# Performance work log

Measured on AMD Instinct MI355X. Metric: run time of the kernel, lower is better.

## Reference

```python
import jax, jax.numpy as jnp
import numpy as np

B, N, S, K = 32, 2048, 64, 128   # clouds, pts/cloud, fps centers (ratio=64/2048), max neighbors
R = 0.2                          # radius ball-query
SLOPE = 0.2                      # LeakyReLU negative slope
C_CONV = [3, 64, 128, 512]       # PointConv local nn
D_FEAT = 512


def leaky(x):
    return jnp.where(x >= 0, x, SLOPE * x)


def _init_linear(key, din, dout):
    kw, kb = jax.random.split(key)
    lim = 1.0 / np.sqrt(din)
    W = jax.random.uniform(kw, (din, dout), minval=-lim, maxval=lim, dtype=jnp.float32)
    b = jax.random.uniform(kb, (dout,), minval=-lim, maxval=lim, dtype=jnp.float32)
    return W, b


def setup_inputs() -> dict:
    key = jax.random.key(0)
    ks = jax.random.split(key, 6)
    pos = jax.random.uniform(ks[0], (B * N, 3), dtype=jnp.float32)
    batch = (jnp.arange(B * N, dtype=jnp.int32) // N)
    W1, b1 = _init_linear(ks[1], 3, 64)
    W2, b2 = _init_linear(ks[2], 64, 128)
    W3, b3 = _init_linear(ks[3], 128, 512)
    W4, b4 = _init_linear(ks[4], D_FEAT + 3, 512)
    W5, b5 = _init_linear(ks[5], 512, 1024)
    return {"pos": pos, "batch": batch,
            "W1": W1, "b1": b1, "W2": W2, "b2": b2, "W3": W3, "b3": b3,
            "W4": W4, "b4": b4, "W5": W5, "b5": b5}


def _fps_one(p):
    """Deterministic farthest point sampling on one cloud p:[N,3] -> idx:[S]."""
    d0 = jnp.sum((p - p[0]) ** 2, axis=-1)

    def step(dists, _):
        nxt = jnp.argmax(dists).astype(jnp.int32)
        dists = jnp.minimum(dists, jnp.sum((p - p[nxt]) ** 2, axis=-1))
        return dists, nxt

    _, rest = jax.lax.scan(step, d0, None, length=S - 1)
    return jnp.concatenate([jnp.zeros((1,), jnp.int32), rest])


def _encoder(pos, W1, b1, W2, b2, W3, b3, W4, b4, W5, b5):
    pts = pos.reshape(B, N, 3)
    idx = jax.vmap(_fps_one)(pts)                                   # [B,S] local fps indices
    centers = jnp.take_along_axis(pts, idx[:, :, None], axis=1)     # [B,S,3]

    # radius ball query (first-by-index up to K neighbors, like torch_cluster cap)
    d2 = jnp.sum((centers[:, :, None, :] - pts[:, None, :, :]) ** 2, axis=-1)  # [B,S,N]
    inball = d2 < R * R
    keys = jnp.where(inball, jnp.arange(N, dtype=jnp.int32)[None, None, :], N)
    nbr = jnp.sort(keys, axis=-1)[:, :, :K]                          # [B,S,K]
    valid = nbr < N
    nbr = jnp.where(valid, nbr, 0)

    # PointConv: gather relative positions -> MLP -> masked max aggregation
    nbr_pos = jnp.take_along_axis(pts[:, None, :, :], nbr[..., None], axis=2)  # [B,S,K,3]
    rel = nbr_pos - centers[:, :, None, :]
    h = leaky(rel @ W1 + b1)
    h = leaky(h @ W2 + b2)
    h = leaky(h @ W3 + b3)                                           # [B,S,K,512]
    h = jnp.where(valid[..., None], h, -jnp.inf)
    feat = jnp.max(h, axis=2)                                        # [B,S,512] (self always in ball)

    g = jnp.concatenate([feat, centers], axis=-1).reshape(B * S, D_FEAT + 3)
    g = leaky(g @ W4 + b4)
    out = g @ W5 + b5                                                # [B*S,1024]
    mean, logvar = out[:, :512], out[:, 512:]
    std = jnp.exp(0.5 * logvar)

    # global edge indices (x_idx = neighbor point id, y_idx = center id), -1 padded
    x_idx = jnp.where(valid, nbr + jnp.arange(B, dtype=jnp.int32)[:, None, None] * N, -1).reshape(-1)
    y_idx = jnp.where(valid, jnp.arange(B * S, dtype=jnp.int32).reshape(B, S, 1), -1).reshape(-1)
    return mean, std, x_idx, y_idx


def reference(pos, batch, W1, b1, W2, b2, W3, b3, W4, b4, W5, b5):
    # batch is implied by the fixed [B,N] layout (sorted, equal-size clouds)
    return _encoder(pos, W1, b1, W2, b2, W3, b3, W4, b4, W5, b5)
```

## Files before the change

kernel.cpp:

```cpp
#include <hip/hip_runtime.h>
#include <hip/hip_bf16.h>

#define NB 32
#define NP 2048
#define NS 64
#define NK 128

#define MEAN_OFF 0
#define STD_OFF  1048576
#define XIDX_OFF 2097152
#define YIDX_OFF 2359296

#define GA_LD 576

typedef __attribute__((ext_vector_type(4)))  short s4;
typedef __attribute__((ext_vector_type(8)))  short short8;
typedef __attribute__((ext_vector_type(16))) float f32x16;

static __device__ __forceinline__ float leaky(float x){ return x >= 0.0f ? x : 0.2f * x; }

static __device__ __forceinline__ unsigned short bf16u(float v){
    __hip_bfloat16 h = __float2bfloat16(v);
    return *(unsigned short*)&h;
}

static __device__ __forceinline__ unsigned cvtpk(float a, float b){
    unsigned d;
    asm("v_cvt_pk_bf16_f32 %0, %1, %2" : "=v"(d) : "v"(a), "v"(b));
    return d;
}
static __device__ __forceinline__ void plswap(unsigned &a, unsigned &b){
    asm volatile("v_permlane32_swap_b32 %0, %1" : "+v"(a), "+v"(b));
}

static __device__ __forceinline__ float d2s(float ax,float ay,float az,float bx,float by,float bz){
    float dx = __fsub_rn(ax,bx), dy = __fsub_rn(ay,by), dz = __fsub_rn(az,bz);
    return __fadd_rn(__fadd_rn(__fmul_rn(dx,dx),__fmul_rn(dy,dy)),__fmul_rn(dz,dz));
}

__global__ __launch_bounds__(256) void fps_prep_kernel(const float* __restrict__ pos,
                                                       float* __restrict__ centersWs,
                                                       const float* __restrict__ W2,
                                                       const float* __restrict__ W3,
                                                       const float* __restrict__ W4,
                                                       const float* __restrict__ W5,
                                                       __hip_bfloat16* __restrict__ W2T,
                                                       __hip_bfloat16* __restrict__ W3T,
                                                       __hip_bfloat16* __restrict__ W4T,
                                                       __hip_bfloat16* __restrict__ W5T)
{
    if (blockIdx.x >= NB) {
        int g = (blockIdx.x - NB)*256 + threadIdx.x;
        if (g < 65536) {
            int c = g >> 7, i = g & 127;
            int byte = c*256 + ((i*2) ^ ((c&15)<<4));
            W3T[byte>>1] = __float2bfloat16(W3[(size_t)i*512 + c]);
        }
        if (g < 8192) {
            int i = g >> 6, j = g & 63;
            W2T[g] = __float2bfloat16(W2[(size_t)j*128 + i]);
        }
        for (int e = g; e < 512*GA_LD; e += 131072) {
            int n = e / GA_LD, k = e - n*GA_LD;
            float v = (k < 515) ? W4[(size_t)k*512 + n] : 0.0f;
            W4T[e] = __float2bfloat16(v);
        }
        for (int e = g; e < 1024*512; e += 131072) {
            int n = e >> 9, k = e & 511;
            W5T[e] = __float2bfloat16(W5[(size_t)k*1024 + n]);
        }
        return;
    }

    int b = blockIdx.x;
    int t = threadIdx.x;
    __shared__ float px[NP], py[NP], pz[NP];
    __shared__ float redv[2][4];
    __shared__ int   redi[2][4];

    const float* pb = pos + (size_t)b * NP * 3;
    for (int n = t; n < NP; n += 256) {
        px[n] = pb[n*3+0]; py[n] = pb[n*3+1]; pz[n] = pb[n*3+2];
    }
    __syncthreads();

    float p0x = px[0], p0y = py[0], p0z = pz[0];
    float dl[8];
    #pragma unroll
    for (int q = 0; q < 8; q++) {
        int n = t + q*256;
        dl[q] = d2s(px[n],py[n],pz[n], p0x,p0y,p0z);
    }
    if (t == 0) {
        centersWs[(b*NS)*3+0] = p0x;
        centersWs[(b*NS)*3+1] = p0y;
        centersWs[(b*NS)*3+2] = p0z;
    }

    int w = t >> 6;
    for (int s = 1; s < NS; s++) {
        float bv = -1.0f; int bi = 0;
        #pragma unroll
        for (int q = 0; q < 8; q++) {
            int n = t + q*256;
            if (dl[q] > bv) { bv = dl[q]; bi = n; }
        }
        #pragma unroll
        for (int m = 32; m > 0; m >>= 1) {
            float ov = __shfl_xor(bv, m);
            int   oi = __shfl_xor(bi, m);
            if (ov > bv || (ov == bv && oi < bi)) { bv = ov; bi = oi; }
        }
        if ((t & 63) == 0) { redv[s&1][w] = bv; redi[s&1][w] = bi; }
        __syncthreads();
        float v = redv[s&1][0]; int j = redi[s&1][0];
        #pragma unroll
        for (int k = 1; k < 4; k++) {
            if (redv[s&1][k] > v || (redv[s&1][k] == v && redi[s&1][k] < j)) { v = redv[s&1][k]; j = redi[s&1][k]; }
        }
        float cx = px[j], cy = py[j], cz = pz[j];
        if (t == 0) {
            centersWs[(b*NS+s)*3+0] = cx;
            centersWs[(b*NS+s)*3+1] = cy;
            centersWs[(b*NS+s)*3+2] = cz;
        }
        #pragma unroll
        for (int q = 0; q < 8; q++) {
            int n = t + q*256;
            dl[q] = fminf(dl[q], d2s(px[n],py[n],pz[n], cx,cy,cz));
        }
    }
}

__global__ __launch_bounds__(256, 4) void ball_mlp_kernel(
    const float* __restrict__ pos,
    const float* __restrict__ W1, const float* __restrict__ b1,
    const float* __restrict__ b2, const float* __restrict__ b3,
    const __hip_bfloat16* __restrict__ W2Tp,
    const __hip_bfloat16* __restrict__ W3Tp,
    const float* __restrict__ centersWs,
    float* __restrict__ out,
    __hip_bfloat16* __restrict__ gAb)
{
    __shared__ char smem[37392];
    char*  h1s  = smem;
    float* relL = (float*)(smem + 32768);
    int*   nbL  = (int*)(smem + 32768);
    float* b2s  = (float*)(smem + 34816);
    float* b3s  = (float*)(smem + 35328);
    int*   cntW4= (int*)(smem + 37376);

    const short* W2T  = (const short*)W2Tp;
    const char*  W3Tb = (const char*)W3Tp;

    int r = blockIdx.x, b = r >> 6, tid = threadIdx.x;
    int l = tid & 63, w = tid >> 6;
    int l31 = l & 31;
    int hsel = l >> 5;
    int jsel8 = hsel * 8;
    int colsel = hsel * 16;

#define STAGE_W3(CH, DST)                                                                              \
    {                                                                                                  \
        const char* _s = W3Tb + (CH)*8192 + w*2048 + l*16;                                             \
        char* _d = (DST) + w*2048;                                                                     \
        __builtin_amdgcn_global_load_lds((const __attribute__((address_space(1))) void*)(_s),          \
                                         (__attribute__((address_space(3))) void*)(_d), 16, 0, 0);     \
        __builtin_amdgcn_global_load_lds((const __attribute__((address_space(1))) void*)(_s + 1024),   \
                                         (__attribute__((address_space(3))) void*)(_d + 1024), 16, 0, 0); \
    }

    STAGE_W3(0, smem + 16384);
    STAGE_W3(1, smem + 24576);

    float cx = centersWs[r*3+0], cy = centersWs[r*3+1], cz = centersWs[r*3+2];

    const float* pb = pos + (size_t)b * NP * 3;
    {
        int myCnt = 0;
        #pragma unroll
        for (int c = 0; c < 8; c++) {
            int n = w*512 + c*64 + l;
            float x = pb[n*3+0], y = pb[n*3+1], z = pb[n*3+2];
            bool in = d2s(cx,cy,cz, x,y,z) < 0.04f;
            unsigned long long m = __ballot(in);
            int before = __popcll(m & ((1ull << l) - 1ull));
            int p = myCnt + before;
            if (in && p < NK) nbL[w*NK + p] = n;
            myCnt += (int)__popcll(m);
        }
        if (l == 0) cntW4[w] = myCnt;
    }
    b3s[tid] = b3[tid];
    b3s[tid + 256] = b3[tid + 256];
    __syncthreads();

    int c0 = cntW4[0], c1 = cntW4[1], c2 = cntW4[2], c3 = cntW4[3];
    int cnt = c0 + c1 + c2 + c3;
    cnt = cnt > NK ? NK : cnt;

    int nv = 0;
    if (tid < NK) {
        bool valid = tid < cnt;
        int seg = 0, off = 0;
        if (tid >= c0)           { seg = 1; off = c0; }
        if (tid >= c0 + c1)      { seg = 2; off = c0 + c1; }
        if (tid >= c0 + c1 + c2) { seg = 3; off = c0 + c1 + c2; }
        if (valid) nv = nbL[seg*NK + (tid - off)];
        out[XIDX_OFF + r*NK + tid] = valid ? (float)(nv + b*NP) : -1.0f;
        out[YIDX_OFF + r*NK + tid] = valid ? (float)r : -1.0f;
    }
    __syncthreads();

    if (tid < NK) {
        const float* pp = pb + (size_t)nv*3;
        relL[tid*4+0] = pp[0] - cx;
        relL[tid*4+1] = pp[1] - cy;
        relL[tid*4+2] = pp[2] - cz;
        relL[tid*4+3] = 0.0f;
        b2s[tid] = b2[tid];
    }
    __syncthreads();

    {
        int jg = (tid & 15) * 4;
        float4 w0 = *(const float4*)&W1[jg];
        float4 w1 = *(const float4*)&W1[64 + jg];
        float4 w2 = *(const float4*)&W1[128 + jg];
        float4 bb = *(const float4*)&b1[jg];
        #pragma unroll
        for (int e = 0; e < 8; e++) {
            int k = (tid >> 4) + e*16;
            float4 r4 = *(const float4*)&relL[k*4];
            s4 pk;
            pk[0] = (short)bf16u(leaky(bb.x + r4.x*w0.x + r4.y*w1.x + r4.z*w2.x));
            pk[1] = (short)bf16u(leaky(bb.y + r4.x*w0.y + r4.y*w1.y + r4.z*w2.y));
            pk[2] = (short)bf16u(leaky(bb.z + r4.x*w0.z + r4.y*w1.z + r4.z*w2.z));
            pk[3] = (short)bf16u(leaky(bb.w + r4.x*w0.w + r4.y*w1.w + r4.z*w2.w));
            *(s4*)(h1s + k*128 + ((jg*2) ^ ((k&7)<<4))) = pk;
        }
    }
    __syncthreads();

    short8 a3[8];
    {
        int kcol = w*32 + l31;
        short8 bh[4];
        #pragma unroll
        for (int ks = 0; ks < 4; ks++) {
            int bc = ks*32 + colsel;
            bh[ks] = *(short8*)(h1s + kcol*128 + (bc ^ ((kcol&7)<<4)));
        }
        #pragma unroll
        for (int it = 0; it < 4; it++) {
            short8 aWf[4];
            #pragma unroll
            for (int ks = 0; ks < 4; ks++)
                aWf[ks] = *(const short8*)(W2T + (it*32 + l31)*64 + ks*16 + jsel8);
            f32x16 acc;
            #pragma unroll
            for (int q = 0; q < 16; q++) acc[q] = 0.f;
            #pragma unroll
            for (int ks = 0; ks < 4; ks++)
                acc = __builtin_amdgcn_mfma_f32_32x32x16_bf16(aWf[ks], bh[ks], acc, 0, 0, 0);
            int ibase = it*32 + 4*hsel;
            #pragma unroll
            for (int g = 0; g < 4; g++) {
                float4 bb = *(const float4*)&b2s[ibase + g*8];
                acc[g*4+0] = leaky(acc[g*4+0] + bb.x);
                acc[g*4+1] = leaky(acc[g*4+1] + bb.y);
                acc[g*4+2] = leaky(acc[g*4+2] + bb.z);
                acc[g*4+3] = leaky(acc[g*4+3] + bb.w);
            }
            #pragma unroll
            for (int hf = 0; hf < 2; hf++) {
                unsigned A0 = cvtpk(acc[hf*8+0], acc[hf*8+1]);
                unsigned A1 = cvtpk(acc[hf*8+2], acc[hf*8+3]);
                unsigned B0 = cvtpk(acc[hf*8+4], acc[hf*8+5]);
                unsigned B1 = cvtpk(acc[hf*8+6], acc[hf*8+7]);
                plswap(A0, B0);
                plswap(A1, B1);
                union { unsigned u[4]; short8 s; } f;
                f.u[0] = A0; f.u[1] = A1; f.u[2] = B0; f.u[3] = B1;
                a3[2*it + hf] = f.s;
            }
        }
    }
    __syncthreads();

    STAGE_W3(2, smem);
    STAGE_W3(3, smem + 8192);

    int kb0 = w*32 + 4*hsel;
    float mred[16];
    #pragma unroll
    for (int t = 0; t < 16; t++) {
        if (t <= 13)      { asm volatile("s_waitcnt vmcnt(4)" ::: "memory"); }
        else if (t == 14) { asm volatile("s_waitcnt vmcnt(2)" ::: "memory"); }
        else              { asm volatile("s_waitcnt vmcnt(0)" ::: "memory"); }
        __builtin_amdgcn_sched_barrier(0);
        __builtin_amdgcn_s_barrier();
        __builtin_amdgcn_sched_barrier(0);

        if (t >= 1 && t + 3 < 16) {
            char* nbuf = smem + 8192*((t+1)&3);
            STAGE_W3(t+3, nbuf);
        }
        __builtin_amdgcn_sched_barrier(0);

        char* buf = smem + 8192*((t+2)&3);
        f32x16 acc;
        #pragma unroll
        for (int q = 0; q < 16; q++) acc[q] = 0.f;
        #pragma unroll
        for (int ks = 0; ks < 8; ks++) {
            int bc = ks*32 + colsel;
            short8 bv = *(short8*)(buf + l31*256 + (bc ^ ((l31&15)<<4)));
            acc = __builtin_amdgcn_mfma_f32_32x32x16_bf16(a3[ks], bv, acc, 0, 0, 0);
        }
        float m = -INFINITY;
        #pragma unroll
        for (int reg = 0; reg < 16; reg++) {
            int kloc = (reg&3) + 8*(reg>>2);
            if (kb0 + kloc < cnt) m = fmaxf(m, acc[reg]);
        }
        m = fmaxf(m, __shfl_xor(m, 32));
        mred[t] = m;
        __builtin_amdgcn_sched_barrier(0);
    }

    float* redf = (float*)(smem + 16384);
    if (l < 32) {
        #pragma unroll
        for (int t = 0; t < 16; t++)
            redf[w*512 + t*32 + l31] = mred[t];
    }
    __syncthreads();
    #pragma unroll
    for (int e = 0; e < 2; e++) {
        int c = tid + e*256;
        float m = fmaxf(fmaxf(redf[c], redf[512 + c]), fmaxf(redf[1024 + c], redf[1536 + c]));
        gAb[(size_t)r*GA_LD + c] = __float2bfloat16(leaky(m + b3s[c]));
    }
    if (tid < 64) {
        float v = 0.0f;
        if (tid == 0) v = cx; else if (tid == 1) v = cy; else if (tid == 2) v = cz;
        gAb[(size_t)r*GA_LD + 512 + tid] = __float2bfloat16(v);
    }
#undef STAGE_W3
}

__global__ __launch_bounds__(256) void fc1_kernel(const __hip_bfloat16* __restrict__ gAb,
                                                  const __hip_bfloat16* __restrict__ W4T,
                                                  const float* __restrict__ b4,
                                                  __hip_bfloat16* __restrict__ g2b)
{
    __shared__ char smem[16384];
    char* As = smem;
    char* Bs = smem + 8192;

    int bx = blockIdx.x & 7;
    int by = blockIdx.x >> 3;
    int tid = threadIdx.x;
    int l = tid & 63, w = tid >> 6;
    int wm = w & 1, wn = w >> 1;
    int colsel = (l >> 5) * 16;

    f32x16 acc;
    #pragma unroll
    for (int q = 0; q < 16; q++) acc[q] = 0.f;

    int ra = wm*32 + (l & 31);
    int rn = wn*32 + (l & 31);

    for (int kb = 0; kb < GA_LD; kb += 64) {
        #pragma unroll
        for (int it = 0; it < 2; it++) {
            int e = it*256 + tid;
            int row = e >> 3, seg = e & 7;
            short8 va = *(const short8*)(gAb + (size_t)(by*64 + row)*GA_LD + kb + seg*8);
            *(short8*)(As + row*128 + ((seg*16) ^ ((row&7)<<4))) = va;
            short8 vb = *(const short8*)(W4T + (size_t)(bx*64 + row)*GA_LD + kb + seg*8);
            *(short8*)(Bs + row*128 + ((seg*16) ^ ((row&7)<<4))) = vb;
        }
        __syncthreads();
        #pragma unroll
        for (int ks = 0; ks < 4; ks++) {
            int bc = ks*32 + colsel;
            short8 av = *(short8*)(As + ra*128 + (bc ^ ((ra&7)<<4)));
            short8 bv = *(short8*)(Bs + rn*128 + (bc ^ ((rn&7)<<4)));
            acc = __builtin_amdgcn_mfma_f32_32x32x16_bf16(av, bv, acc, 0, 0, 0);
        }
        __syncthreads();
    }

    int col = bx*64 + wn*32 + (l & 31);
    float bcol = b4[col];
    int rbase = by*64 + wm*32 + 4*(l>>5);
    #pragma unroll
    for (int reg = 0; reg < 16; reg++) {
        int row = rbase + (reg&3) + 8*(reg>>2);
        g2b[(size_t)row*512 + col] = __float2bfloat16(leaky(acc[reg] + bcol));
    }
}

__global__ __launch_bounds__(256) void fc2_kernel(const __hip_bfloat16* __restrict__ g2b,
                                                  const __hip_bfloat16* __restrict__ W5T,
                                                  const float* __restrict__ b5,
                                                  float* __restrict__ out)
{
    __shared__ char smem[16384];
    char* As = smem;
    char* Bs = smem + 8192;

    int bx = blockIdx.x & 15;
    int by = blockIdx.x >> 4;
    int tid = threadIdx.x;
    int l = tid & 63, w = tid >> 6;
    int wm = w & 1, wn = w >> 1;
    int colsel = (l >> 5) * 16;

    f32x16 acc;
    #pragma unroll
    for (int q = 0; q < 16; q++) acc[q] = 0.f;

    int ra = wm*32 + (l & 31);
    int rn = wn*32 + (l & 31);

    for (int kb = 0; kb < 512; kb += 64) {
        #pragma unroll
        for (int it = 0; it < 2; it++) {
            int e = it*256 + tid;
            int row = e >> 3, seg = e & 7;
            short8 va = *(const short8*)(g2b + (size_t)(by*64 + row)*512 + kb + seg*8);
            *(short8*)(As + row*128 + ((seg*16) ^ ((row&7)<<4))) = va;
            short8 vb = *(const short8*)(W5T + (size_t)(bx*64 + row)*512 + kb + seg*8);
            *(short8*)(Bs + row*128 + ((seg*16) ^ ((row&7)<<4))) = vb;
        }
        __syncthreads();
        #pragma unroll
        for (int ks = 0; ks < 4; ks++) {
            int bc = ks*32 + colsel;
            short8 av = *(short8*)(As + ra*128 + (bc ^ ((ra&7)<<4)));
            short8 bv = *(short8*)(Bs + rn*128 + (bc ^ ((rn&7)<<4)));
            acc = __builtin_amdgcn_mfma_f32_32x32x16_bf16(av, bv, acc, 0, 0, 0);
        }
        __syncthreads();
    }

    int col = bx*64 + wn*32 + (l & 31);
    float bcol = b5[col];
    int rbase = by*64 + wm*32 + 4*(l>>5);
    #pragma unroll
    for (int reg = 0; reg < 16; reg++) {
        int row = rbase + (reg&3) + 8*(reg>>2);
        float v = acc[reg] + bcol;
        if (col < 512) {
            out[MEAN_OFF + (size_t)row*512 + col] = v;
        } else {
            out[STD_OFF + (size_t)row*512 + (col - 512)] = expf(0.5f*v);
        }
    }
}

extern "C" void kernel_launch(void* const* d_in, const int* in_sizes, int n_in,
                              void* d_out, int out_size, void* d_ws, size_t ws_size,
                              hipStream_t stream) {
    const float* pos = (const float*)d_in[0];
    const float* W1  = (const float*)d_in[2];
    const float* b1  = (const float*)d_in[3];
    const float* W2  = (const float*)d_in[4];
    const float* b2  = (const float*)d_in[5];
    const float* W3  = (const float*)d_in[6];
    const float* b3  = (const float*)d_in[7];
    const float* W4  = (const float*)d_in[8];
    const float* b4  = (const float*)d_in[9];
    const float* W5  = (const float*)d_in[10];
    const float* b5  = (const float*)d_in[11];
    float* out = (float*)d_out;

    char* ws = (char*)d_ws;
    float* centersWs = (float*)(ws);
    __hip_bfloat16* gAb = (__hip_bfloat16*)(ws + 1081344);
    __hip_bfloat16* g2b = (__hip_bfloat16*)(ws + 3440640);
    __hip_bfloat16* W2T = (__hip_bfloat16*)(ws + 5537792);
    __hip_bfloat16* W3T = (__hip_bfloat16*)(ws + 5554176);
    __hip_bfloat16* W4T = (__hip_bfloat16*)(ws + 5685248);
    __hip_bfloat16* W5T = (__hip_bfloat16*)(ws + 6275072);

    hipLaunchKernelGGL(fps_prep_kernel, dim3(NB + 512), dim3(256), 0, stream,
                       pos, centersWs, W2, W3, W4, W5, W2T, W3T, W4T, W5T);
    hipLaunchKernelGGL(ball_mlp_kernel, dim3(NB*NS), dim3(256), 0, stream,
                       pos, W1,b1, b2,b3, W2T, W3T, centersWs, out, gAb);
    hipLaunchKernelGGL(fc1_kernel, dim3(256), dim3(256), 0, stream, gAb, W4T, b4, g2b);
    hipLaunchKernelGGL(fc2_kernel, dim3(512), dim3(256), 0, stream, g2b, W5T, b5, out);
}
```

Baseline: 151.6 us.

## Tile weight transposes through LDS and streamline FPS argmax loop

The weight-conversion blocks now transpose W2-W5 in 64x64 tiles staged through shared memory, so both the global reads and the global writes are coalesced instead of strided. This also cuts the number of prep blocks. The FPS loop fuses the distance update with the per-thread argmax and carries the candidate point's coordinates through the shuffle reduction, which removes a dependent LDS lookup per step. Centers are buffered in LDS and written out once at the end. The cost is more shuffles per reduction step and more shared-memory use in the FPS blocks.

```diff
diff --git a/kernel.cpp b/kernel.cpp
--- a/kernel.cpp
+++ b/kernel.cpp
@@ -50,24 +50,57 @@
                                                        __hip_bfloat16* __restrict__ W5T)
 {
     if (blockIdx.x >= NB) {
-        int g = (blockIdx.x - NB)*256 + threadIdx.x;
-        if (g < 65536) {
-            int c = g >> 7, i = g & 127;
-            int byte = c*256 + ((i*2) ^ ((c&15)<<4));
-            W3T[byte>>1] = __float2bfloat16(W3[(size_t)i*512 + c]);
-        }
-        if (g < 8192) {
-            int i = g >> 6, j = g & 63;
-            W2T[g] = __float2bfloat16(W2[(size_t)j*128 + i]);
-        }
-        for (int e = g; e < 512*GA_LD; e += 131072) {
-            int n = e / GA_LD, k = e - n*GA_LD;
-            float v = (k < 515) ? W4[(size_t)k*512 + n] : 0.0f;
-            W4T[e] = __float2bfloat16(v);
-        }
-        for (int e = g; e < 1024*512; e += 131072) {
-            int n = e >> 9, k = e & 511;
-            W5T[e] = __float2bfloat16(W5[(size_t)k*1024 + n]);
+        __shared__ float tl[64][65];
+        int tb = blockIdx.x - NB;
+        int t = threadIdx.x;
+        int tr = t >> 6;
+        int tc = t & 63;
+        if (tb < 72) {
+            int kt = tb >> 3, nt = tb & 7;
+            int k0 = kt*64, n0 = nt*64;
+            #pragma unroll
+            for (int it = 0; it < 16; it++) {
+                int k = k0 + tr + it*4;
+                tl[tr + it*4][tc] = (k < 515) ? W4[(size_t)k*512 + n0 + tc] : 0.0f;
+            }
+            __syncthreads();
+            #pragma unroll
+            for (int it = 0; it < 16; it++) {
+                int nl = tr + it*4;
+                W4T[(size_t)(n0 + nl)*GA_LD + k0 + tc] = __float2bfloat16(tl[tc][nl]);
+            }
+        } else if (tb < 200) {
+            int q = tb - 72;
+            int kt = q >> 4, nt = q & 15;
+            int k0 = kt*64, n0 = nt*64;
+            #pragma unroll
+            for (int it = 0; it < 16; it++)
+                tl[tr + it*4][tc] = W5[(size_t)(k0 + tr + it*4)*1024 + n0 + tc];
+            __syncthreads();
+            #pragma unroll
+            for (int it = 0; it < 16; it++) {
+                int nl = tr + it*4;
+                W5T[(size_t)(n0 + nl)*512 + k0 + tc] = __float2bfloat16(tl[tc][nl]);
+            }
+        } else if (tb < 216) {
+            int q = tb - 200;
+            int i0 = (q >> 3)*64, c0 = (q & 7)*64;
+            #pragma unroll
+            for (int it = 0; it < 16; it++)
+                tl[tr + it*4][tc] = W3[(size_t)(i0 + tr + it*4)*512 + c0 + tc];
+            __syncthreads();
+            #pragma unroll
+            for (int it = 0; it < 16; it++) {
+                int c = c0 + tr + it*4;
+                int i = i0 + tc;
+                int byte = c*256 + ((i*2) ^ ((c&15)<<4));
+                *(unsigned short*)((char*)W3T + byte) = bf16u(tl[tc][tr + it*4]);
+            }
+        } else {
+            for (int e = t; e < 8192; e += 256) {
+                int i = e & 127, j = e >> 7;
+                W2T[i*64 + j] = __float2bfloat16(W2[(size_t)j*128 + i]);
+            }
         }
         return;
     }
@@ -75,8 +108,9 @@
     int b = blockIdx.x;
     int t = threadIdx.x;
     __shared__ float px[NP], py[NP], pz[NP];
-    __shared__ float redv[2][4];
+    __shared__ float redv[2][4], redx[2][4], redy[2][4], redz[2][4];
     __shared__ int   redi[2][4];
+    __shared__ float cbuf[NS*3];
 
     const float* pb = pos + (size_t)b * NP * 3;
     for (int n = t; n < NP; n += 256) {
@@ -85,51 +119,58 @@
     __syncthreads();
 
     float p0x = px[0], p0y = py[0], p0z = pz[0];
+    if (t == 0) { cbuf[0] = p0x; cbuf[1] = p0y; cbuf[2] = p0z; }
+
     float dl[8];
+    float bv = -1.0f; int bi = 0;
     #pragma unroll
     for (int q = 0; q < 8; q++) {
         int n = t + q*256;
         dl[q] = d2s(px[n],py[n],pz[n], p0x,p0y,p0z);
-    }
-    if (t == 0) {
-        centersWs[(b*NS)*3+0] = p0x;
-        centersWs[(b*NS)*3+1] = p0y;
-        centersWs[(b*NS)*3+2] = p0z;
-    }
+        if (dl[q] > bv) { bv = dl[q]; bi = n; }
+    }
+    float lx = px[bi], ly = py[bi], lz = pz[bi];
 
     int w = t >> 6;
     for (int s = 1; s < NS; s++) {
-        float bv = -1.0f; int bi = 0;
-        #pragma unroll
-        for (int q = 0; q < 8; q++) {
-            int n = t + q*256;
-            if (dl[q] > bv) { bv = dl[q]; bi = n; }
-        }
         #pragma unroll
         for (int m = 32; m > 0; m >>= 1) {
             float ov = __shfl_xor(bv, m);
             int   oi = __shfl_xor(bi, m);
-            if (ov > bv || (ov == bv && oi < bi)) { bv = ov; bi = oi; }
-        }
-        if ((t & 63) == 0) { redv[s&1][w] = bv; redi[s&1][w] = bi; }
+            float ox = __shfl_xor(lx, m);
+            float oy = __shfl_xor(ly, m);
+            float oz = __shfl_xor(lz, m);
+            if (ov > bv || (ov == bv && oi < bi)) { bv = ov; bi = oi; lx = ox; ly = oy; lz = oz; }
+        }
+        int s1 = s & 1;
+        if ((t & 63) == 0) {
+            redv[s1][w] = bv; redi[s1][w] = bi;
+            redx[s1][w] = lx; redy[s1][w] = ly; redz[s1][w] = lz;
+        }
         __syncthreads();
-        float v = redv[s&1][0]; int j = redi[s&1][0];
+        float v = redv[s1][0]; int j = redi[s1][0];
+        float cx = redx[s1][0], cy = redy[s1][0], cz = redz[s1][0];
         #pragma unroll
         for (int k = 1; k < 4; k++) {
-            if (redv[s&1][k] > v || (redv[s&1][k] == v && redi[s&1][k] < j)) { v = redv[s&1][k]; j = redi[s&1][k]; }
-        }
-        float cx = px[j], cy = py[j], cz = pz[j];
-        if (t == 0) {
-            centersWs[(b*NS+s)*3+0] = cx;
-            centersWs[(b*NS+s)*3+1] = cy;
-            centersWs[(b*NS+s)*3+2] = cz;
-        }
+            if (redv[s1][k] > v || (redv[s1][k] == v && redi[s1][k] < j)) {
+                v = redv[s1][k]; j = redi[s1][k];
+                cx = redx[s1][k]; cy = redy[s1][k]; cz = redz[s1][k];
+            }
+        }
+        if (t == 0) { cbuf[s*3+0] = cx; cbuf[s*3+1] = cy; cbuf[s*3+2] = cz; }
+        bv = -1.0f; bi = 0;
         #pragma unroll
         for (int q = 0; q < 8; q++) {
             int n = t + q*256;
-            dl[q] = fminf(dl[q], d2s(px[n],py[n],pz[n], cx,cy,cz));
-        }
-    }
+            float nd = fminf(dl[q], d2s(px[n],py[n],pz[n], cx,cy,cz));
+            dl[q] = nd;
+            if (nd > bv) { bv = nd; bi = n; }
+        }
+        lx = px[bi]; ly = py[bi]; lz = pz[bi];
+    }
+    __syncthreads();
+    for (int e = t; e < NS*3; e += 256)
+        centersWs[(size_t)b*NS*3 + e] = cbuf[e];
 }
 
 __global__ __launch_bounds__(256, 4) void ball_mlp_kernel(
@@ -488,7 +529,7 @@
     __hip_bfloat16* W4T = (__hip_bfloat16*)(ws + 5685248);
     __hip_bfloat16* W5T = (__hip_bfloat16*)(ws + 6275072);
 
-    hipLaunchKernelGGL(fps_prep_kernel, dim3(NB + 512), dim3(256), 0, stream,
+    hipLaunchKernelGGL(fps_prep_kernel, dim3(NB + 217), dim3(256), 0, stream,
                        pos, centersWs, W2, W3, W4, W5, W2T, W3T, W4T, W5T);
     hipLaunchKernelGGL(ball_mlp_kernel, dim3(NB*NS), dim3(256), 0, stream,
                        pos, W1,b1, b2,b3, W2T, W3T, centersWs, out, gAb);
```

After: 156.6 us. 3.3% more time.
